# Kernel optimization log

Hardware: AMD Instinct MI355X
Metric: run time of the kernel (lower is better)

Reference implementation:

```python
import jax, jax.numpy as jnp
import numpy as np

TOPK_RATIOS = (0.67, 0.75, 0.8)


def setup_inputs() -> dict:
    key = jax.random.key(0)
    k0, k1, k2 = jax.random.split(key, 3)
    B, L, S, H, E, D = 4, 2048, 2048, 8, 64, 64
    queries = jax.random.normal(k0, (B, L, H, E), dtype=jnp.float32)
    keys = jax.random.normal(k1, (B, S, H, E), dtype=jnp.float32)
    values = jax.random.normal(k2, (B, S, H, D), dtype=jnp.float32)
    attn_weights = jnp.ones((len(TOPK_RATIOS),), dtype=jnp.float32)  # nn.Parameter(ones)
    attn_mask = jnp.zeros((1,), dtype=bool)  # unused by the module
    return {"queries": queries, "keys": keys, "values": values,
            "attn_weights": attn_weights, "attn_mask": attn_mask}


def reference(queries, keys, values, attn_weights, attn_mask):
    # queries: [B,L,H,E], keys: [B,S,H,E], values: [B,S,H,D]
    B, L, H, E = queries.shape
    S = keys.shape[1]
    scale = 1.0 / np.sqrt(E)  # self.scale is None -> 1/sqrt(E)
    scores = jnp.einsum('blhe,bshe->bhls', queries, keys) * scale  # [B,H,L,S]
    out = jnp.zeros(queries.shape[:3] + (values.shape[-1],), dtype=scores.dtype)
    for i, ratio in enumerate(TOPK_RATIOS):
        k = int(S * ratio)
        topv = jax.lax.top_k(scores, k)[0]            # sorted descending
        kth = topv[..., -1:]                           # k-th largest per row
        # mask==0 -> -inf, then softmax over S (ties at threshold are measure-zero)
        masked = jnp.where(scores >= kth, scores, -jnp.inf)
        attn = jax.nn.softmax(masked, axis=-1)         # dropout = identity (eval)
        out = out + jnp.einsum('bhls,bshd->blhd', attn, values) * attn_weights[i]
    return out
```

## Files before the change

### kernel.cpp

```cpp
#include <hip/hip_runtime.h>
#include <hip/hip_fp16.h>

typedef _Float16 f16x8 __attribute__((ext_vector_type(8)));
typedef float f32x4 __attribute__((ext_vector_type(4)));

#define KSEL0 1372u
#define KSEL1 1536u
#define KSEL2 1638u
#define WSC 16.0f

__device__ __forceinline__ unsigned ou16_of(unsigned hb) {
  return hb ^ ((hb & 0x8000u) ? 0xFFFFu : 0x8000u);
}
__device__ __forceinline__ unsigned ou16_inv(unsigned ou) {
  return (ou & 0x8000u) ? (ou ^ 0x8000u) : (ou ^ 0xFFFFu);
}
__device__ __forceinline__ unsigned pk2(float a, float b) {
  auto h = __builtin_amdgcn_cvt_pkrtz(a, b);
  return __builtin_bit_cast(unsigned, h);
}
__device__ __forceinline__ unsigned shflx(unsigned v, int m) {
  return (unsigned)__shfl_xor((int)v, m, 64);
}

__device__ __forceinline__ unsigned sel_digit_s(const unsigned* histw, unsigned k,
                                                int lane, int shift) {
  uint4 hr = ((const uint4*)histw)[lane];
  unsigned hx = (hr.x >> shift) & 0xFFFFu;
  unsigned hy = (hr.y >> shift) & 0xFFFFu;
  unsigned hz = (hr.z >> shift) & 0xFFFFu;
  unsigned hw_ = (hr.w >> shift) & 0xFFFFu;
  unsigned s4 = hx + hy + hz + hw_;
  unsigned p = s4;
  #pragma unroll
  for (int off = 1; off < 64; off <<= 1) {
    int sl = lane + off;
    unsigned t = (unsigned)__shfl((int)p, sl < 64 ? sl : lane, 64);
    p += (sl < 64) ? t : 0u;
  }
  unsigned a3 = p - s4;
  unsigned a2 = a3 + hw_;
  unsigned a1 = a2 + hz;
  unsigned a0 = a1 + hy;
  int d = -1; unsigned nk = 0;
  if (a3 < k && a3 + hw_ >= k)      { d = 4*lane+3; nk = k - a3; }
  else if (a2 < k && a2 + hz >= k)  { d = 4*lane+2; nk = k - a2; }
  else if (a1 < k && a1 + hy >= k)  { d = 4*lane+1; nk = k - a1; }
  else if (a0 < k && a0 + hx >= k)  { d = 4*lane+0; nk = k - a0; }
  unsigned long long mb = __ballot(d >= 0);
  int src = __ffsll(mb) - 1;
  unsigned pack = ((unsigned)d << 16) | nk;
  return (unsigned)__shfl((int)pack, src, 64);
}

extern "C" __global__ __launch_bounds__(256)
void prep_k(const float* __restrict__ K, unsigned short* __restrict__ Kh) {
  int idx = blockIdx.x * 256 + threadIdx.x;
  int ec = idx & 7;
  int s  = (idx >> 3) & 2047;
  int bh = idx >> 14;
  int b = bh >> 3, h = bh & 7;
  const float* src = K + (((size_t)b * 2048 + s) * 8 + h) * 64 + ec * 8;
  float4 a = *(const float4*)src;
  float4 c = *(const float4*)(src + 4);
  uint4 val = { pk2(a.x, a.y), pk2(a.z, a.w), pk2(c.x, c.y), pk2(c.z, c.w) };
  *(uint4*)(Kh + (size_t)idx * 8) = val;
}

extern "C" __global__ __launch_bounds__(256)
void prep_v(const float* __restrict__ V, unsigned short* __restrict__ Vt) {
  const int tid  = threadIdx.x;
  const int w    = tid >> 6;
  const int lane = tid & 63;
  const int u_   = lane >> 4;
  const int dq   = (lane >> 2) & 3;
  const int r_   = lane & 3;
  const unsigned selv = (lane & 1) ? 0x03020706u : 0x05040100u;

  int bh = blockIdx.x >> 4;
  int s0 = (blockIdx.x & 15) * 128;
  int b = bh >> 3, h = bh & 7;
  const float* Vb = V + ((size_t)b * 2048 * 8 + h) * 64;
  unsigned short* Vo = Vt + (size_t)bh * 64 * 2048;

  #pragma unroll
  for (int sp = 0; sp < 2; ++sp) {
    #pragma unroll
    for (int p = 0; p < 4; ++p) {
      int sl = w * 32 + sp * 16 + u_ * 4;
      int sg = s0 + sl + r_;
      int d0 = p * 16 + dq * 4;
      float4 f = *(const float4*)(Vb + (size_t)sg * 512 + d0);
      unsigned lo = pk2(f.x, f.y), hi = pk2(f.z, f.w);
      unsigned tlo = shflx(lo, 1), thi = shflx(hi, 1);
      lo = __builtin_amdgcn_perm(tlo, lo, selv);
      hi = __builtin_amdgcn_perm(thi, hi, selv);
      unsigned t2lo = shflx(lo, 2), t2hi = shflx(hi, 2);
      unsigned Aw = (lane & 2) ? t2hi : lo;
      unsigned Bw = (lane & 2) ? hi   : t2lo;
      int d = d0 + r_;
      uint2 wv = {Aw, Bw};
      *(uint2*)(Vo + (size_t)d * 2048 + s0 + sl) = wv;
    }
  }
}

extern "C" __global__ __launch_bounds__(512, 4)
void nma_kernel(const float* __restrict__ Q, const unsigned short* __restrict__ Kh,
                const unsigned short* __restrict__ Vt, const float* __restrict__ AW,
                float* __restrict__ Out)
{
  __shared__ __align__(16) char lds[81920];
  unsigned* work = (unsigned*)(lds + 65536);

  const int tid  = threadIdx.x;
  const int w    = tid >> 6;
  const int lane = tid & 63;
  const int g    = lane >> 4;
  const int lx   = lane & 15;

  int bid = blockIdx.x;
  int lb  = (bid & 7) * 512 + (bid >> 3);
  int bh  = lb >> 7;
  int b   = bh >> 3, hh = bh & 7;
  int l0  = (lb & 127) << 4;

  const float* Qb = Q + (((size_t)b * 2048 + l0) * 8 + hh) * 64;
  const unsigned short* Khb = Kh + (size_t)bh * 2048 * 64;
  const unsigned short* Vtb = Vt + (size_t)bh * 64 * 2048;

  {
    uint4 z4 = {0u,0u,0u,0u};
    uint4* p = (uint4*)work;
    p[tid] = z4;
    p[tid + 512] = z4;
  }

  union FU { f16x8 v; unsigned u[4]; };
  FU qa0, qa1;
  {
    const float* qp = Qb + (size_t)lx * 512 + g * 8;
    float4 a = *(const float4*)(qp);
    float4 c = *(const float4*)(qp + 4);
    qa0.u[0] = pk2(a.x*0.125f, a.y*0.125f); qa0.u[1] = pk2(a.z*0.125f, a.w*0.125f);
    qa0.u[2] = pk2(c.x*0.125f, c.y*0.125f); qa0.u[3] = pk2(c.z*0.125f, c.w*0.125f);
    a = *(const float4*)(qp + 32);
    c = *(const float4*)(qp + 36);
    qa1.u[0] = pk2(a.x*0.125f, a.y*0.125f); qa1.u[1] = pk2(a.z*0.125f, a.w*0.125f);
    qa1.u[2] = pk2(c.x*0.125f, c.y*0.125f); qa1.u[3] = pk2(c.z*0.125f, c.w*0.125f);
  }
  __syncthreads();

  const unsigned swl = (((unsigned)(lx & 7)) << 4) | (((unsigned)(lx & 8)) << 3);
  unsigned* hq = work + lx * 256;
  #pragma unroll 2
  for (int t = 0; t < 16; ++t) {
    int s0 = (t * 8 + w) * 16;
    const unsigned short* kp = Khb + (size_t)(s0 + lx) * 64 + g * 8;
    f16x8 kb0 = *(const f16x8*)(kp);
    f16x8 kb1 = *(const f16x8*)(kp + 32);
    f32x4 acc = {0.f, 0.f, 0.f, 0.f};
    acc = __builtin_amdgcn_mfma_f32_16x16x32_f16(kb0, qa0.v, acc, 0, 0, 0);
    acc = __builtin_amdgcn_mfma_f32_16x16x32_f16(kb1, qa1.v, acc, 0, 0, 0);
    unsigned u0 = pk2(acc[0], acc[1]);
    unsigned u1 = pk2(acc[2], acc[3]);
    uint2 wv = {u0, u1};
    *(uint2*)(lds + lx * 4096 + (((unsigned)(s0 * 2 + g * 8)) ^ swl)) = wv;
    atomicAdd(&hq[ou16_of(u0 & 0xFFFFu) >> 8], 1u);
    atomicAdd(&hq[ou16_of(u0 >> 16) >> 8], 1u);
    atomicAdd(&hq[ou16_of(u1 & 0xFFFFu) >> 8], 1u);
    atomicAdd(&hq[ou16_of(u1 >> 16) >> 8], 1u);
  }
  __syncthreads();

  const float aw0 = AW[0], aw1 = AW[1], aw2 = AW[2];

  unsigned d0a[2], d1a[2], d2a[2], k0a[2], k1a[2], k2a[2];
  float ma[2];
  #pragma unroll
  for (int rr = 0; rr < 2; ++rr) {
    int q = 2 * w + rr;
    const unsigned* hw1 = work + q * 256;
    unsigned p0 = sel_digit_s(hw1, KSEL0, lane, 0);
    unsigned p1 = sel_digit_s(hw1, KSEL1, lane, 0);
    unsigned p2 = sel_digit_s(hw1, KSEL2, lane, 0);
    d0a[rr] = p0 >> 16; k0a[rr] = p0 & 0xFFFFu;
    d1a[rr] = p1 >> 16; k1a[rr] = p1 & 0xFFFFu;
    d2a[rr] = p2 >> 16; k2a[rr] = p2 & 0xFFFFu;
    uint4 hb = ((const uint4*)hw1)[lane];
    int md = hb.w ? lane*4+3 : hb.z ? lane*4+2 : hb.y ? lane*4+1 : (hb.x ? lane*4 : -1);
    #pragma unroll
    for (int off = 1; off < 64; off <<= 1) md = max(md, __shfl_xor(md, off, 64));
    ma[rr] = __half2float(__ushort_as_half((unsigned short)ou16_inv((unsigned)md * 256u + 255u)));
  }

  unsigned* hw2 = work + w * 512;
  #pragma unroll 1
  for (int rr = 0; rr < 2; ++rr) {
    int q = 2 * w + rr;
    const unsigned swq = (((unsigned)(q & 7)) << 4) | (((unsigned)(q & 8)) << 3);
    char* rowp = lds + q * 4096;
    for (int i = lane; i < 512; i += 64) hw2[i] = 0u;
    unsigned D0 = d0a[rr], D1 = d1a[rr], D2 = d2a[rr];
    for (int it = 0; it < 4; ++it) {
      uint4 dv = *(const uint4*)(rowp + (((unsigned)(it * 1024 + lane * 16)) ^ swq));
      unsigned ws[4] = {dv.x, dv.y, dv.z, dv.w};
      #pragma unroll
      for (int p = 0; p < 4; ++p) {
        #pragma unroll
        for (int hp = 0; hp < 2; ++hp) {
          unsigned bits = (ws[p] >> (hp * 16)) & 0xFFFFu;
          unsigned ou = ou16_of(bits);
          unsigned hi = ou >> 8, lo = ou & 255u;
          unsigned add = (hi == D0 ? 1u : 0u) | (hi == D1 ? 0x10000u : 0u);
          if (add) atomicAdd(&hw2[lo], add);
          if (hi == D2) atomicAdd(&hw2[256 + lo], 1u);
        }
      }
    }
    unsigned T1o = (D0 << 8) | (sel_digit_s(hw2,       k0a[rr], lane, 0)  >> 16);
    unsigned T2o = (D1 << 8) | (sel_digit_s(hw2,       k1a[rr], lane, 16) >> 16);
    unsigned T3o = (D2 << 8) | (sel_digit_s(hw2 + 256, k2a[rr], lane, 0)  >> 16);
    float m = ma[rr];
    float z1 = 0.f, z2 = 0.f, z3 = 0.f;
    for (int it = 0; it < 4; ++it) {
      char* ap = rowp + (((unsigned)(it * 1024 + lane * 16)) ^ swq);
      uint4 dv = *(const uint4*)ap;
      unsigned ws[4] = {dv.x, dv.y, dv.z, dv.w};
      uint4 nv;
      unsigned no[4];
      #pragma unroll
      for (int p = 0; p < 4; ++p) {
        unsigned b0 = ws[p] & 0xFFFFu, b1 = ws[p] >> 16;
        float s0 = __half2float(__ushort_as_half((unsigned short)b0));
        float s1 = __half2float(__ushort_as_half((unsigned short)b1));
        float e0 = __expf(s0 - m), e1 = __expf(s1 - m);
        unsigned o0 = ou16_of(b0), o1 = ou16_of(b1);
        if (o0 >= T3o) z3 += e0;
        if (o0 >= T2o) z2 += e0;
        if (o0 >= T1o) z1 += e0;
        if (o1 >= T3o) z3 += e1;
        if (o1 >= T2o) z2 += e1;
        if (o1 >= T1o) z1 += e1;
        no[p] = pk2(e0, e1);
      }
      nv.x = no[0]; nv.y = no[1]; nv.z = no[2]; nv.w = no[3];
      *(uint4*)ap = nv;
    }
    #pragma unroll
    for (int off = 1; off < 64; off <<= 1) {
      z1 += __shfl_xor(z1, off, 64);
      z2 += __shfl_xor(z2, off, 64);
      z3 += __shfl_xor(z3, off, 64);
    }
    float A3 = aw2 / z3;
    float A2 = aw1 / z2 + A3;
    float A1 = aw0 / z1 + A2;
    A1 *= WSC; A2 *= WSC; A3 *= WSC;
    float T1f = __half2float(__ushort_as_half((unsigned short)ou16_inv(T1o)));
    float T2f = __half2float(__ushort_as_half((unsigned short)ou16_inv(T2o)));
    float T3f = __half2float(__ushort_as_half((unsigned short)ou16_inv(T3o)));
    unsigned e1b = pk2(__expf(T1f - m), 0.f) & 0xFFFFu;
    unsigned e2b = pk2(__expf(T2f - m), 0.f) & 0xFFFFu;
    unsigned e3b = pk2(__expf(T3f - m), 0.f) & 0xFFFFu;
    for (int it = 0; it < 4; ++it) {
      char* ap = rowp + (((unsigned)(it * 1024 + lane * 16)) ^ swq);
      uint4 dv = *(const uint4*)ap;
      unsigned ws[4] = {dv.x, dv.y, dv.z, dv.w};
      uint4 nv;
      unsigned no[4];
      #pragma unroll
      for (int p = 0; p < 4; ++p) {
        unsigned b0 = ws[p] & 0xFFFFu, b1 = ws[p] >> 16;
        float e0 = __half2float(__ushort_as_half((unsigned short)b0));
        float e1 = __half2float(__ushort_as_half((unsigned short)b1));
        float c0 = (b0 >= e1b) ? A1 : (b0 >= e2b) ? A2 : (b0 >= e3b) ? A3 : 0.f;
        float c1 = (b1 >= e1b) ? A1 : (b1 >= e2b) ? A2 : (b1 >= e3b) ? A3 : 0.f;
        no[p] = pk2(e0 * c0, e1 * c1);
      }
      nv.x = no[0]; nv.y = no[1]; nv.z = no[2]; nv.w = no[3];
      *(uint4*)ap = nv;
    }
  }
  __syncthreads();

  f32x4 oacc = {0.f, 0.f, 0.f, 0.f};
  const int dt = (w >> 1) * 16;
  const int sh = w & 1;
  const unsigned short* vp = Vtb + (size_t)(dt + lx) * 2048 + sh * 1024 + g * 8;
  const char* bp = lds + lx * 4096;

  #pragma unroll 8
  for (int kc = 0; kc < 32; ++kc) {
    f16x8 av = *(const f16x8*)(vp + kc * 32);
    unsigned sb = (unsigned)((sh * 1024 + kc * 32 + g * 8) * 2);
    f16x8 bv = *(const f16x8*)(bp + (sb ^ swl));
    oacc = __builtin_amdgcn_mfma_f32_16x16x32_f16(av, bv, oacc, 0, 0, 0);
  }

  float* pbuf = (float*)work;
  *(f32x4*)(pbuf + w * 256 + lx * 16 + g * 4) = oacc;
  __syncthreads();
  if (w < 4) {
    const float* pa = pbuf + (2 * w) * 256 + lx * 16 + g * 4;
    float4 ra = *(const float4*)pa;
    float4 rb = *(const float4*)(pa + 256);
    float* op = Out + (((size_t)b * 2048 + l0 + lx) * 8 + hh) * 64 + w * 16 + g * 4;
    float4 ov = { (ra.x + rb.x) * (1.f/WSC), (ra.y + rb.y) * (1.f/WSC),
                  (ra.z + rb.z) * (1.f/WSC), (ra.w + rb.w) * (1.f/WSC) };
    *(float4*)op = ov;
  }
}

extern "C" void kernel_launch(void* const* d_in, const int* in_sizes, int n_in,
                              void* d_out, int out_size, void* d_ws, size_t ws_size,
                              hipStream_t stream) {
  (void)in_sizes; (void)n_in; (void)out_size; (void)ws_size;
  const float* Q  = (const float*)d_in[0];
  const float* K  = (const float*)d_in[1];
  const float* V  = (const float*)d_in[2];
  const float* AW = (const float*)d_in[3];
  unsigned short* Kh = (unsigned short*)d_ws;
  unsigned short* Vt = (unsigned short*)((char*)d_ws + 8388608);
  prep_k<<<dim3(2048), dim3(256), 0, stream>>>(K, Kh);
  prep_v<<<dim3(512),  dim3(256), 0, stream>>>(V, Vt);
  nma_kernel<<<dim3(4096), dim3(512), 0, stream>>>(Q, Kh, Vt, AW, (float*)d_out);
}
```

Before: 379.3 us.

## Keep score tiles in registers and process selection passes in MFMA-fragment layout

Scores stay in 32 registers per thread after the QK MFMA instead of being written to LDS and re-read row by row. The second-level histogram, exp and normaliser passes run on the register copies, with thresholds and partial sums exchanged through small LDS buffers and extra block barriers. The prefix scan is shared across the three k-selections, and the second histogram is interleaved so one 8-word load feeds all three. Only the final weighted probabilities go to LDS for the PV MFMA, removing several full LDS sweeps at the cost of higher register pressure, which may reduce occupancy.

```diff
diff --git a/kernel.cpp b/kernel.cpp
--- a/kernel.cpp
+++ b/kernel.cpp
@@ -23,14 +23,7 @@
   return (unsigned)__shfl_xor((int)v, m, 64);
 }
 
-__device__ __forceinline__ unsigned sel_digit_s(const unsigned* histw, unsigned k,
-                                                int lane, int shift) {
-  uint4 hr = ((const uint4*)histw)[lane];
-  unsigned hx = (hr.x >> shift) & 0xFFFFu;
-  unsigned hy = (hr.y >> shift) & 0xFFFFu;
-  unsigned hz = (hr.z >> shift) & 0xFFFFu;
-  unsigned hw_ = (hr.w >> shift) & 0xFFFFu;
-  unsigned s4 = hx + hy + hz + hw_;
+__device__ __forceinline__ unsigned suffix64(unsigned s4, int lane) {
   unsigned p = s4;
   #pragma unroll
   for (int off = 1; off < 64; off <<= 1) {
@@ -38,7 +31,12 @@
     unsigned t = (unsigned)__shfl((int)p, sl < 64 ? sl : lane, 64);
     p += (sl < 64) ? t : 0u;
   }
-  unsigned a3 = p - s4;
+  return p;
+}
+__device__ __forceinline__ unsigned pick_digit(unsigned tail, unsigned hx, unsigned hy,
+                                               unsigned hz, unsigned hw_, unsigned k, int lane) {
+  unsigned s4 = hx + hy + hz + hw_;
+  unsigned a3 = tail - s4;
   unsigned a2 = a3 + hw_;
   unsigned a1 = a2 + hz;
   unsigned a0 = a1 + hy;
@@ -111,7 +109,11 @@
                 float* __restrict__ Out)
 {
   __shared__ __align__(16) char lds[81920];
-  unsigned* work = (unsigned*)(lds + 65536);
+  unsigned* hist1 = (unsigned*)(lds + 65536);
+  unsigned* h2    = (unsigned*)lds;
+  char* dkbuf = lds + 32768;
+  char* tmbuf = lds + 33024;
+  char* zbuf  = lds + 33280;
 
   const int tid  = threadIdx.x;
   const int w    = tid >> 6;
@@ -131,9 +133,10 @@
 
   {
     uint4 z4 = {0u,0u,0u,0u};
-    uint4* p = (uint4*)work;
-    p[tid] = z4;
-    p[tid + 512] = z4;
+    uint4* p1 = (uint4*)hist1;
+    p1[tid] = z4; p1[tid + 512] = z4;
+    uint4* p2 = (uint4*)lds;
+    p2[tid] = z4; p2[tid + 512] = z4; p2[tid + 1024] = z4; p2[tid + 1536] = z4;
   }
 
   union FU { f16x8 v; unsigned u[4]; };
@@ -151,9 +154,9 @@
   }
   __syncthreads();
 
-  const unsigned swl = (((unsigned)(lx & 7)) << 4) | (((unsigned)(lx & 8)) << 3);
-  unsigned* hq = work + lx * 256;
-  #pragma unroll 2
+  unsigned sreg[32];
+  unsigned* hq = hist1 + lx * 256;
+  #pragma unroll
   for (int t = 0; t < 16; ++t) {
     int s0 = (t * 8 + w) * 16;
     const unsigned short* kp = Khb + (size_t)(s0 + lx) * 64 + g * 8;
@@ -164,8 +167,8 @@
     acc = __builtin_amdgcn_mfma_f32_16x16x32_f16(kb1, qa1.v, acc, 0, 0, 0);
     unsigned u0 = pk2(acc[0], acc[1]);
     unsigned u1 = pk2(acc[2], acc[3]);
-    uint2 wv = {u0, u1};
-    *(uint2*)(lds + lx * 4096 + (((unsigned)(s0 * 2 + g * 8)) ^ swl)) = wv;
+    sreg[2*t]   = u0;
+    sreg[2*t+1] = u1;
     atomicAdd(&hq[ou16_of(u0 & 0xFFFFu) >> 8], 1u);
     atomicAdd(&hq[ou16_of(u0 >> 16) >> 8], 1u);
     atomicAdd(&hq[ou16_of(u1 & 0xFFFFu) >> 8], 1u);
@@ -175,112 +178,138 @@
 
   const float aw0 = AW[0], aw1 = AW[1], aw2 = AW[2];
 
-  unsigned d0a[2], d1a[2], d2a[2], k0a[2], k1a[2], k2a[2];
-  float ma[2];
   #pragma unroll
   for (int rr = 0; rr < 2; ++rr) {
     int q = 2 * w + rr;
-    const unsigned* hw1 = work + q * 256;
-    unsigned p0 = sel_digit_s(hw1, KSEL0, lane, 0);
-    unsigned p1 = sel_digit_s(hw1, KSEL1, lane, 0);
-    unsigned p2 = sel_digit_s(hw1, KSEL2, lane, 0);
-    d0a[rr] = p0 >> 16; k0a[rr] = p0 & 0xFFFFu;
-    d1a[rr] = p1 >> 16; k1a[rr] = p1 & 0xFFFFu;
-    d2a[rr] = p2 >> 16; k2a[rr] = p2 & 0xFFFFu;
-    uint4 hb = ((const uint4*)hw1)[lane];
+    uint4 hb = ((const uint4*)(hist1 + q * 256))[lane];
+    unsigned tail = suffix64(hb.x + hb.y + hb.z + hb.w, lane);
+    unsigned p0 = pick_digit(tail, hb.x, hb.y, hb.z, hb.w, KSEL0, lane);
+    unsigned p1 = pick_digit(tail, hb.x, hb.y, hb.z, hb.w, KSEL1, lane);
+    unsigned p2 = pick_digit(tail, hb.x, hb.y, hb.z, hb.w, KSEL2, lane);
     int md = hb.w ? lane*4+3 : hb.z ? lane*4+2 : hb.y ? lane*4+1 : (hb.x ? lane*4 : -1);
     #pragma unroll
     for (int off = 1; off < 64; off <<= 1) md = max(md, __shfl_xor(md, off, 64));
-    ma[rr] = __half2float(__ushort_as_half((unsigned short)ou16_inv((unsigned)md * 256u + 255u)));
-  }
-
-  unsigned* hw2 = work + w * 512;
-  #pragma unroll 1
+    float m = __half2float(__ushort_as_half((unsigned short)ou16_inv((unsigned)md * 256u + 255u)));
+    if (lane == 0) {
+      uint4 dk = { (p0 >> 16) | ((p1 >> 16) << 8) | ((p2 >> 16) << 16),
+                   (p0 & 0xFFFFu) | ((p1 & 0xFFFFu) << 16),
+                   (p2 & 0xFFFFu),
+                   __float_as_uint(m) };
+      *(uint4*)(dkbuf + q * 16) = dk;
+    }
+  }
+  __syncthreads();
+
+  uint4 dk = *(const uint4*)(dkbuf + lx * 16);
+  const unsigned D0 = dk.x & 255u, D1 = (dk.x >> 8) & 255u, D2 = (dk.x >> 16) & 255u;
+  const unsigned k0r = dk.y & 0xFFFFu, k1r = dk.y >> 16, k2r = dk.z;
+  const float m = __uint_as_float(dk.w);
+  unsigned* h2r = h2 + lx * 512;
+  #pragma unroll
+  for (int i = 0; i < 32; ++i) {
+    unsigned uu = sreg[i];
+    #pragma unroll
+    for (int hp = 0; hp < 2; ++hp) {
+      unsigned bits = (uu >> (hp * 16)) & 0xFFFFu;
+      unsigned ou = ou16_of(bits);
+      unsigned hi = ou >> 8, lo = ou & 255u;
+      unsigned add = (hi == D0 ? 1u : 0u) | (hi == D1 ? 0x10000u : 0u);
+      if (add) atomicAdd(&h2r[lo * 2], add);
+      if (hi == D2) atomicAdd(&h2r[lo * 2 + 1], 1u);
+    }
+  }
+  __syncthreads();
+
+  #pragma unroll
   for (int rr = 0; rr < 2; ++rr) {
     int q = 2 * w + rr;
-    const unsigned swq = (((unsigned)(q & 7)) << 4) | (((unsigned)(q & 8)) << 3);
-    char* rowp = lds + q * 4096;
-    for (int i = lane; i < 512; i += 64) hw2[i] = 0u;
-    unsigned D0 = d0a[rr], D1 = d1a[rr], D2 = d2a[rr];
-    for (int it = 0; it < 4; ++it) {
-      uint4 dv = *(const uint4*)(rowp + (((unsigned)(it * 1024 + lane * 16)) ^ swq));
-      unsigned ws[4] = {dv.x, dv.y, dv.z, dv.w};
-      #pragma unroll
-      for (int p = 0; p < 4; ++p) {
-        #pragma unroll
-        for (int hp = 0; hp < 2; ++hp) {
-          unsigned bits = (ws[p] >> (hp * 16)) & 0xFFFFu;
-          unsigned ou = ou16_of(bits);
-          unsigned hi = ou >> 8, lo = ou & 255u;
-          unsigned add = (hi == D0 ? 1u : 0u) | (hi == D1 ? 0x10000u : 0u);
-          if (add) atomicAdd(&hw2[lo], add);
-          if (hi == D2) atomicAdd(&hw2[256 + lo], 1u);
-        }
-      }
+    const unsigned* hr = h2 + q * 512 + lane * 8;
+    uint4 v0 = *(const uint4*)hr;
+    uint4 v1 = *(const uint4*)(hr + 4);
+    uint4 dkq = *(const uint4*)(dkbuf + q * 16);
+    unsigned Dq0 = dkq.x & 255u, Dq1 = (dkq.x >> 8) & 255u, Dq2 = (dkq.x >> 16) & 255u;
+    unsigned hx = v0.x & 0xFFFFu, hy = v0.z & 0xFFFFu, hz = v1.x & 0xFFFFu, hw_ = v1.z & 0xFFFFu;
+    unsigned t0 = suffix64(hx + hy + hz + hw_, lane);
+    unsigned T1o = (Dq0 << 8) | (pick_digit(t0, hx, hy, hz, hw_, dkq.y & 0xFFFFu, lane) >> 16);
+    hx = v0.x >> 16; hy = v0.z >> 16; hz = v1.x >> 16; hw_ = v1.z >> 16;
+    unsigned t1 = suffix64(hx + hy + hz + hw_, lane);
+    unsigned T2o = (Dq1 << 8) | (pick_digit(t1, hx, hy, hz, hw_, dkq.y >> 16, lane) >> 16);
+    hx = v0.y; hy = v0.w; hz = v1.y; hw_ = v1.w;
+    unsigned t2 = suffix64(hx + hy + hz + hw_, lane);
+    unsigned T3o = (Dq2 << 8) | (pick_digit(t2, hx, hy, hz, hw_, dkq.z, lane) >> 16);
+    if (lane == 0) {
+      uint4 tm = {T1o, T2o, T3o, 0u};
+      *(uint4*)(tmbuf + q * 16) = tm;
     }
-    unsigned T1o = (D0 << 8) | (sel_digit_s(hw2,       k0a[rr], lane, 0)  >> 16);
-    unsigned T2o = (D1 << 8) | (sel_digit_s(hw2,       k1a[rr], lane, 16) >> 16);
-    unsigned T3o = (D2 << 8) | (sel_digit_s(hw2 + 256, k2a[rr], lane, 0)  >> 16);
-    float m = ma[rr];
-    float z1 = 0.f, z2 = 0.f, z3 = 0.f;
-    for (int it = 0; it < 4; ++it) {
-      char* ap = rowp + (((unsigned)(it * 1024 + lane * 16)) ^ swq);
-      uint4 dv = *(const uint4*)ap;
-      unsigned ws[4] = {dv.x, dv.y, dv.z, dv.w};
-      uint4 nv;
-      unsigned no[4];
-      #pragma unroll
-      for (int p = 0; p < 4; ++p) {
-        unsigned b0 = ws[p] & 0xFFFFu, b1 = ws[p] >> 16;
-        float s0 = __half2float(__ushort_as_half((unsigned short)b0));
-        float s1 = __half2float(__ushort_as_half((unsigned short)b1));
-        float e0 = __expf(s0 - m), e1 = __expf(s1 - m);
-        unsigned o0 = ou16_of(b0), o1 = ou16_of(b1);
-        if (o0 >= T3o) z3 += e0;
-        if (o0 >= T2o) z2 += e0;
-        if (o0 >= T1o) z1 += e0;
-        if (o1 >= T3o) z3 += e1;
-        if (o1 >= T2o) z2 += e1;
-        if (o1 >= T1o) z1 += e1;
-        no[p] = pk2(e0, e1);
-      }
-      nv.x = no[0]; nv.y = no[1]; nv.z = no[2]; nv.w = no[3];
-      *(uint4*)ap = nv;
-    }
-    #pragma unroll
-    for (int off = 1; off < 64; off <<= 1) {
-      z1 += __shfl_xor(z1, off, 64);
-      z2 += __shfl_xor(z2, off, 64);
-      z3 += __shfl_xor(z3, off, 64);
-    }
-    float A3 = aw2 / z3;
-    float A2 = aw1 / z2 + A3;
-    float A1 = aw0 / z1 + A2;
-    A1 *= WSC; A2 *= WSC; A3 *= WSC;
-    float T1f = __half2float(__ushort_as_half((unsigned short)ou16_inv(T1o)));
-    float T2f = __half2float(__ushort_as_half((unsigned short)ou16_inv(T2o)));
-    float T3f = __half2float(__ushort_as_half((unsigned short)ou16_inv(T3o)));
-    unsigned e1b = pk2(__expf(T1f - m), 0.f) & 0xFFFFu;
-    unsigned e2b = pk2(__expf(T2f - m), 0.f) & 0xFFFFu;
-    unsigned e3b = pk2(__expf(T3f - m), 0.f) & 0xFFFFu;
-    for (int it = 0; it < 4; ++it) {
-      char* ap = rowp + (((unsigned)(it * 1024 + lane * 16)) ^ swq);
-      uint4 dv = *(const uint4*)ap;
-      unsigned ws[4] = {dv.x, dv.y, dv.z, dv.w};
-      uint4 nv;
-      unsigned no[4];
-      #pragma unroll
-      for (int p = 0; p < 4; ++p) {
-        unsigned b0 = ws[p] & 0xFFFFu, b1 = ws[p] >> 16;
-        float e0 = __half2float(__ushort_as_half((unsigned short)b0));
-        float e1 = __half2float(__ushort_as_half((unsigned short)b1));
-        float c0 = (b0 >= e1b) ? A1 : (b0 >= e2b) ? A2 : (b0 >= e3b) ? A3 : 0.f;
-        float c1 = (b1 >= e1b) ? A1 : (b1 >= e2b) ? A2 : (b1 >= e3b) ? A3 : 0.f;
-        no[p] = pk2(e0 * c0, e1 * c1);
-      }
-      nv.x = no[0]; nv.y = no[1]; nv.z = no[2]; nv.w = no[3];
-      *(uint4*)ap = nv;
-    }
+  }
+  __syncthreads();
+
+  uint4 tm = *(const uint4*)(tmbuf + lx * 16);
+  const unsigned T1o = tm.x, T2o = tm.y, T3o = tm.z;
+  float z1 = 0.f, z2 = 0.f, z3 = 0.f;
+  #pragma unroll
+  for (int i = 0; i < 32; ++i) {
+    unsigned uu = sreg[i];
+    unsigned b0 = uu & 0xFFFFu, b1 = uu >> 16;
+    float s0 = __half2float(__ushort_as_half((unsigned short)b0));
+    float s1 = __half2float(__ushort_as_half((unsigned short)b1));
+    float e0 = __expf(s0 - m), e1 = __expf(s1 - m);
+    unsigned o0 = ou16_of(b0), o1 = ou16_of(b1);
+    if (o0 >= T3o) z3 += e0;
+    if (o0 >= T2o) z2 += e0;
+    if (o0 >= T1o) z1 += e0;
+    if (o1 >= T3o) z3 += e1;
+    if (o1 >= T2o) z2 += e1;
+    if (o1 >= T1o) z1 += e1;
+    sreg[i] = pk2(e0, e1);
+  }
+  z1 += __uint_as_float(shflx(__float_as_uint(z1), 16));
+  z2 += __uint_as_float(shflx(__float_as_uint(z2), 16));
+  z3 += __uint_as_float(shflx(__float_as_uint(z3), 16));
+  z1 += __uint_as_float(shflx(__float_as_uint(z1), 32));
+  z2 += __uint_as_float(shflx(__float_as_uint(z2), 32));
+  z3 += __uint_as_float(shflx(__float_as_uint(z3), 32));
+  if (g == 0) {
+    float4 zv = {z1, z2, z3, 0.f};
+    *(float4*)(zbuf + (lx * 8 + w) * 16) = zv;
+  }
+  __syncthreads();
+
+  float zs1 = 0.f, zs2 = 0.f, zs3 = 0.f;
+  #pragma unroll
+  for (int ww = 0; ww < 8; ++ww) {
+    float4 zv = *(const float4*)(zbuf + (lx * 8 + ww) * 16);
+    zs1 += zv.x; zs2 += zv.y; zs3 += zv.z;
+  }
+  float A3 = aw2 / zs3;
+  float A2 = aw1 / zs2 + A3;
+  float A1 = aw0 / zs1 + A2;
+  A1 *= WSC; A2 *= WSC; A3 *= WSC;
+  float T1f = __half2float(__ushort_as_half((unsigned short)ou16_inv(T1o)));
+  float T2f = __half2float(__ushort_as_half((unsigned short)ou16_inv(T2o)));
+  float T3f = __half2float(__ushort_as_half((unsigned short)ou16_inv(T3o)));
+  unsigned e1b = pk2(__expf(T1f - m), 0.f) & 0xFFFFu;
+  unsigned e2b = pk2(__expf(T2f - m), 0.f) & 0xFFFFu;
+  unsigned e3b = pk2(__expf(T3f - m), 0.f) & 0xFFFFu;
+  __syncthreads();
+
+  const unsigned swl = (((unsigned)(lx & 7)) << 4) | (((unsigned)(lx & 8)) << 3);
+  #pragma unroll
+  for (int t = 0; t < 16; ++t) {
+    int s0 = (t * 8 + w) * 16;
+    unsigned u0 = sreg[2*t], u1 = sreg[2*t+1];
+    unsigned b0 = u0 & 0xFFFFu, b1 = u0 >> 16;
+    unsigned b2 = u1 & 0xFFFFu, b3 = u1 >> 16;
+    float e0 = __half2float(__ushort_as_half((unsigned short)b0));
+    float e1 = __half2float(__ushort_as_half((unsigned short)b1));
+    float e2 = __half2float(__ushort_as_half((unsigned short)b2));
+    float e3 = __half2float(__ushort_as_half((unsigned short)b3));
+    float c0 = (b0 >= e1b) ? A1 : (b0 >= e2b) ? A2 : (b0 >= e3b) ? A3 : 0.f;
+    float c1 = (b1 >= e1b) ? A1 : (b1 >= e2b) ? A2 : (b1 >= e3b) ? A3 : 0.f;
+    float c2 = (b2 >= e1b) ? A1 : (b2 >= e2b) ? A2 : (b2 >= e3b) ? A3 : 0.f;
+    float c3 = (b3 >= e1b) ? A1 : (b3 >= e2b) ? A2 : (b3 >= e3b) ? A3 : 0.f;
+    uint2 wv = { pk2(e0 * c0, e1 * c1), pk2(e2 * c2, e3 * c3) };
+    *(uint2*)(lds + lx * 4096 + (((unsigned)(s0 * 2 + g * 8)) ^ swl)) = wv;
   }
   __syncthreads();
 
@@ -298,7 +327,7 @@
     oacc = __builtin_amdgcn_mfma_f32_16x16x32_f16(av, bv, oacc, 0, 0, 0);
   }
 
-  float* pbuf = (float*)work;
+  float* pbuf = (float*)hist1;
   *(f32x4*)(pbuf + w * 256 + lx * 16 + g * 4) = oacc;
   __syncthreads();
   if (w < 4) {
```

Result: slower. 489.0 us (+28.9%).
